# Kernel tuning notes

Hardware: AMD Instinct MI355X
Metric: run time of the kernel (lower is better)

Reference implementation:

```python
import jax, jax.numpy as jnp
import numpy as np
import math

B, S = 512, 100
L, U = 50000, 2000
D, LOC_DIM, USER_DIM, TEMP_DIM = 80, 56, 12, 12
NHEAD, DFF = 4, 160


def _pe(seq_len, d):
    pos = np.arange(seq_len, dtype=np.float32)[:, None]
    div = np.exp(np.arange(0, d, 2, dtype=np.float32) * (-math.log(10000.0) / d))
    pe = np.zeros((seq_len, d), dtype=np.float32)
    pe[:, 0::2] = np.sin(pos * div)
    pe[:, 1::2] = np.cos(pos * div)
    return jnp.asarray(pe)


def _ln(x, g, b, eps=1e-5):
    m = x.mean(-1, keepdims=True)
    v = ((x - m) ** 2).mean(-1, keepdims=True)
    return (x - m) * jax.lax.rsqrt(v + eps) * g + b


def setup_inputs():
    key = jax.random.key(0)
    ks = jax.random.split(key, 16)
    f32 = jnp.float32
    def n(k, shape, s):
        return (jax.random.normal(k, shape) * s).astype(f32)
    return {
        'loc_seq': jax.random.randint(ks[0], (B, S), 0, L),
        'user_seq': jax.random.randint(ks[1], (B, S), 0, U),
        'weekday_seq': jax.random.randint(ks[2], (B, S), 0, 7),
        'start_min_seq': (jax.random.uniform(ks[3], (B, S)) * 1440.0).astype(f32),
        'dur_seq': (jax.random.uniform(ks[4], (B, S)) * 120.0).astype(f32),
        'diff_seq': jax.random.randint(ks[5], (B, S), 0, 7),
        'mask': jnp.ones((B, S), dtype=bool),
        'loc_emb': n(ks[6], (L, LOC_DIM), 0.01).at[0].set(0.0),
        'user_emb': n(ks[7], (U, USER_DIM), 0.01).at[0].set(0.0),
        'Wt': n(ks[8], (6, TEMP_DIM), 0.3), 'bt': jnp.zeros((TEMP_DIM,), f32),
        'in_g': jnp.ones((D,), f32), 'in_b': jnp.zeros((D,), f32),
        'Wq': n(ks[9], (D, D), 0.05), 'bq': jnp.zeros((D,), f32),
        'Wk': n(ks[10], (D, D), 0.05), 'bk': jnp.zeros((D,), f32),
        'Wv': n(ks[11], (D, D), 0.05), 'bv': jnp.zeros((D,), f32),
        'Wo': n(ks[12], (D, D), 0.05), 'bo': jnp.zeros((D,), f32),
        'ln1_g': jnp.ones((D,), f32), 'ln1_b': jnp.zeros((D,), f32),
        'W1': n(ks[13], (D, DFF), 0.05), 'b1': jnp.zeros((DFF,), f32),
        'W2': n(ks[14], (DFF, D), 0.05), 'b2': jnp.zeros((D,), f32),
        'ln2_g': jnp.ones((D,), f32), 'ln2_b': jnp.zeros((D,), f32),
        'out_g': jnp.ones((D,), f32), 'out_b': jnp.zeros((D,), f32),
        'Wp': n(ks[15], (D, L), 0.05), 'bp': jnp.zeros((L,), f32),
        'recency_decay': jnp.array(0.62, f32),
        'freq_weight': jnp.array(2.2, f32),
        'history_scale': jnp.array(11.0, f32),
        'model_weight': jnp.array(0.22, f32),
    }


def reference(loc_seq, user_seq, weekday_seq, start_min_seq, dur_seq, diff_seq, mask,
              loc_emb, user_emb, Wt, bt, in_g, in_b,
              Wq, bq, Wk, bk, Wv, bv, Wo, bo, ln1_g, ln1_b,
              W1, b1, W2, b2, ln2_g, ln2_b, out_g, out_b, Wp, bp,
              recency_decay, freq_weight, history_scale, model_weight):
    b, s = loc_seq.shape
    nloc = Wp.shape[1]
    valid = mask.astype(jnp.float32)
    # --- history scores: the torch per-timestep scatter loop, vectorized ---
    t = jnp.arange(s)
    rec_w = recency_decay ** (s - 1 - t).astype(jnp.float32)      # (s,) decay^time_from_end
    bidx = jnp.broadcast_to(jnp.arange(b)[:, None], (b, s))
    recency = jnp.zeros((b, nloc), jnp.float32).at[bidx, loc_seq].max(rec_w[None, :] * valid)
    freq = jnp.zeros((b, nloc), jnp.float32).at[bidx, loc_seq].add(valid)
    freq = freq / jnp.maximum(freq.max(axis=1, keepdims=True), 1.0)
    history_scores = history_scale * (recency + freq_weight * freq)
    # --- embeddings & temporal features ---
    time_rad = start_min_seq / 60.0 / 24.0 * 2.0 * math.pi
    wd_rad = weekday_seq.astype(jnp.float32) / 7.0 * 2.0 * math.pi
    feats = jnp.stack([jnp.sin(time_rad), jnp.cos(time_rad), jnp.log1p(dur_seq) / 8.0,
                       jnp.sin(wd_rad), jnp.cos(wd_rad), diff_seq.astype(jnp.float32) / 7.0], axis=-1)
    x = jnp.concatenate([loc_emb[loc_seq], user_emb[user_seq], feats @ Wt + bt], axis=-1)
    x = _ln(x, in_g, in_b) + _pe(s, x.shape[-1])[None]
    # --- 1-layer post-norm transformer encoder, erf-gelu, eval (no dropout) ---
    dh = D // NHEAD
    q = (x @ Wq + bq).reshape(b, s, NHEAD, dh)
    k = (x @ Wk + bk).reshape(b, s, NHEAD, dh)
    v = (x @ Wv + bv).reshape(b, s, NHEAD, dh)
    scores = jnp.einsum('bqhd,bkhd->bhqk', q, k) / math.sqrt(dh)
    scores = jnp.where(mask[:, None, None, :], scores, -1e9)
    attn = jnp.einsum('bhqk,bkhd->bqhd', jax.nn.softmax(scores, axis=-1), v).reshape(b, s, D)
    x = _ln(x + attn @ Wo + bo, ln1_g, ln1_b)
    x = _ln(x + jax.nn.gelu(x @ W1 + b1, approximate=False) @ W2 + b2, ln2_g, ln2_b)
    # --- gather last valid position ---
    last_idx = mask.sum(axis=1) - 1
    last = jnp.take_along_axis(x, last_idx[:, None, None], axis=1)[:, 0]
    last = _ln(last, out_g, out_b)
    learned = jax.nn.softmax(last @ Wp + bp, axis=1) * nloc
    return history_scores + model_weight * learned
```

## Files before the change

### kernel.cpp

```cpp
#include <hip/hip_runtime.h>
#include <hip/hip_bf16.h>
#include <math.h>

#define B 512
#define S 100
#define L 50000
#define D 80
#define NHEAD 4
#define DH 20
#define DFF 160
#define NTOK (B*S)
#define NTILES 3125

typedef __attribute__((ext_vector_type(8))) short bf16x8v;
typedef __attribute__((ext_vector_type(4))) float f32x4v;
typedef __attribute__((ext_vector_type(4))) unsigned short u16x4;
typedef __attribute__((ext_vector_type(8))) unsigned short u16x8;

__device__ __forceinline__ unsigned short f2bf(float f) {
    unsigned int x = __float_as_uint(f);
    unsigned int r = (x + 0x7FFFu + ((x >> 16) & 1u)) >> 16;
    return (unsigned short)r;
}

__device__ __forceinline__ float bf2f(unsigned short u) {
    return __uint_as_float(((unsigned int)u) << 16);
}

__device__ __forceinline__ float pe_val(int s, int d) {
    int k = d >> 1;
    float ang = (float)s * expf(-0.23025850929940458f * (float)k);
    return (d & 1) ? cosf(ang) : sinf(ang);
}

__global__ __launch_bounds__(256) void pack_all(const float* __restrict__ Wq, const float* __restrict__ Wk,
                        const float* __restrict__ Wv, const float* __restrict__ Wo,
                        const float* __restrict__ W1, const float* __restrict__ W2,
                        unsigned short* __restrict__ U) {
    int bid = blockIdx.x;
    const float* W; int K, N, KT, nt; unsigned short* dst;
    if (bid < 15)      { int mt = bid / 5; nt = bid % 5; W = (mt==0)?Wq:(mt==1)?Wk:Wv; K=80; N=80; KT=3; dst = U + (size_t)bid * 1536; }
    else if (bid < 20) { nt = bid - 15; W = Wo; K=80;  N=80;  KT=3; dst = U + 23040 + (size_t)nt * 1536; }
    else if (bid < 30) { nt = bid - 20; W = W1; K=80;  N=160; KT=3; dst = U + 30720 + (size_t)nt * 1536; }
    else               { nt = bid - 30; W = W2; K=160; N=80;  KT=5; dst = U + 46080 + (size_t)nt * 2560; }
    int total = KT * 512;
    for (int idx = threadIdx.x; idx < total; idx += 256) {
        int j = idx & 7, n = (idx >> 3) & 15, q = (idx >> 7) & 3, kt = idx >> 9;
        int k = kt * 32 + q * 8 + j;
        float val = (k < K) ? W[(size_t)k * N + nt * 16 + n] : 0.f;
        dst[idx] = f2bf(val);
    }
}

__global__ __launch_bounds__(256) void build_x(const int* __restrict__ loc_seq, const int* __restrict__ user_seq,
                        const int* __restrict__ weekday_seq, const float* __restrict__ start_min,
                        const float* __restrict__ dur, const int* __restrict__ diff,
                        const float* __restrict__ loc_emb, const float* __restrict__ user_emb,
                        const float* __restrict__ Wt, const float* __restrict__ bt,
                        const float* __restrict__ in_g, const float* __restrict__ in_b,
                        unsigned short* __restrict__ x) {
    int token = blockIdx.x * 4 + (threadIdx.x >> 6);
    int lane = threadIdx.x & 63;
    int s = token % S;
    int lidx = loc_seq[token];
    int uidx = user_seq[token];
    float tr = start_min[token] * (2.f * (float)M_PI / 1440.f);
    float wd = (float)weekday_seq[token] * (2.f * (float)M_PI / 7.f);
    float f0 = sinf(tr), f1 = cosf(tr);
    float f2 = log1pf(dur[token]) * 0.125f;
    float f3 = sinf(wd), f4 = cosf(wd);
    float f5 = (float)diff[token] * (1.f / 7.f);
    float v1;
    if (lane < 56) v1 = loc_emb[(size_t)lidx * 56 + lane];
    else           v1 = user_emb[(size_t)uidx * 12 + (lane - 56)];
    float v2 = 0.f;
    if (lane < 4) {
        v2 = user_emb[(size_t)uidx * 12 + 8 + lane];
    } else if (lane < 16) {
        int j = lane - 4;
        v2 = bt[j] + f0 * Wt[j] + f1 * Wt[12 + j] + f2 * Wt[24 + j]
                   + f3 * Wt[36 + j] + f4 * Wt[48 + j] + f5 * Wt[60 + j];
    }
    float sum = v1 + v2, sq = v1 * v1 + v2 * v2;
    #pragma unroll
    for (int off = 1; off < 64; off <<= 1) {
        sum += __shfl_xor(sum, off);
        sq  += __shfl_xor(sq,  off);
    }
    float mean = sum * 0.0125f;
    float var = sq * 0.0125f - mean * mean;
    float rstd = rsqrtf(var + 1e-5f);
    x[(size_t)token * D + lane] = f2bf((v1 - mean) * rstd * in_g[lane] + in_b[lane] + pe_val(s, lane));
    if (lane < 16) {
        int d2 = 64 + lane;
        x[(size_t)token * D + d2] = f2bf((v2 - mean) * rstd * in_g[d2] + in_b[d2] + pe_val(s, d2));
    }
}

__global__ __launch_bounds__(512) void qkv_attn_last(const unsigned short* __restrict__ xg,
      const unsigned short* __restrict__ qkvP,
      const float* __restrict__ bq, const float* __restrict__ bk, const float* __restrict__ bv,
      unsigned short* __restrict__ ao_last) {
    __shared__ __align__(16) unsigned short xbf[112 * 96];
    __shared__ __align__(16) unsigned short kls[112 * 128];
    __shared__ __align__(16) unsigned short vt[4 * 32 * 128];
    __shared__ __align__(16) unsigned short qls[16 * 128];
    __shared__ float pls[4 * 112];
    __shared__ float lls[4];
    int tid = threadIdx.x;
    int b = blockIdx.x;
    size_t base = (size_t)b * (S * D);
    f32x4v zz = {0.f, 0.f, 0.f, 0.f};
    f32x4v* k4 = (f32x4v*)kls; f32x4v* v4 = (f32x4v*)vt; f32x4v* q4 = (f32x4v*)qls;
    #pragma unroll
    for (int ii = 0; ii < 4; ++ii) { int i = tid + ii * 512; if (i < 1792) k4[i] = zz; }
    #pragma unroll
    for (int ii = 0; ii < 4; ++ii) v4[tid + ii * 512] = zz;
    if (tid < 256) q4[tid] = zz;
    #pragma unroll
    for (int ii = 0; ii < 4; ++ii) {
        int i = tid + ii * 512;
        if (i < 2000) {
            int row = i / 20, c0 = (i % 20) * 4;
            *(u16x4*)&xbf[row * 96 + c0] = *(const u16x4*)&xg[base + row * 80 + c0];
        }
    }
    unsigned int* xb32 = (unsigned int*)xbf;
    for (int i = tid; i < 576; i += 512) xb32[4800 + i] = 0;
    for (int i = tid; i < 800; i += 512) { int r = i / 8, c = i % 8; xb32[r * 48 + 40 + c] = 0; }
    __syncthreads();
    int w = tid >> 6, lane = tid & 63;
    int qd = lane >> 4, m = lane & 15;
    if (w < 7) {
        int mt = w;
        bf16x8v a[3];
        #pragma unroll
        for (int t = 0; t < 3; ++t)
            a[t] = *(const bf16x8v*)&xbf[(mt * 16 + m) * 96 + t * 32 + qd * 8];
        #pragma unroll
        for (int nt = 0; nt < 15; ++nt) {
            f32x4v acc = {0.f, 0.f, 0.f, 0.f};
            #pragma unroll
            for (int t = 0; t < 3; ++t) {
                bf16x8v bb = *(const bf16x8v*)&qkvP[(((size_t)(nt * 3 + t)) * 4 + qd) * 128 + m * 8];
                acc = __builtin_amdgcn_mfma_f32_16x16x32_bf16(a[t], bb, acc, 0, 0, 0);
            }
            int mat = nt / 5;
            int col80 = nt * 16 + m - mat * 80;
            int h = col80 / 20, dd = col80 % 20;
            const float* bias = (mat == 0) ? bq : (mat == 1) ? bk : bv;
            float bbv = bias[col80];
            float scl = (mat == 0) ? 0.22360679774997896f : 1.f;
            #pragma unroll
            for (int r = 0; r < 4; ++r) {
                int row = mt * 16 + qd * 4 + r;
                unsigned short val = f2bf((acc[r] + bbv) * scl);
                if (mat == 0) {
                    if (row >= 96) qls[(row - 96) * 128 + ((h * 32 + dd) ^ ((row & 7) << 3))] = val;
                } else if (mat == 1) {
                    kls[row * 128 + ((h * 32 + dd) ^ ((row & 7) << 3))] = val;
                } else {
                    vt[h * 4096 + dd * 128 + (row ^ ((dd & 7) << 3))] = val;
                }
            }
        }
    }
    __syncthreads();
    if (w < 4) {
        int hb = w * 32;
        bf16x8v aq = *(const bf16x8v*)&qls[m * 128 + ((hb + qd * 8) ^ ((m & 7) << 3))];
        f32x4v scv[7];
        #pragma unroll
        for (int nt = 0; nt < 7; ++nt) {
            int krow = nt * 16 + m;
            bf16x8v bk_ = *(const bf16x8v*)&kls[krow * 128 + ((hb + qd * 8) ^ ((krow & 7) << 3))];
            f32x4v z = {0.f, 0.f, 0.f, 0.f};
            scv[nt] = __builtin_amdgcn_mfma_f32_16x16x32_bf16(aq, bk_, z, 0, 0, 0);
        }
        float mx = scv[0][3];
        #pragma unroll
        for (int nt = 1; nt < 6; ++nt) mx = fmaxf(mx, scv[nt][3]);
        float s6 = scv[6][3];
        if (m < 4) mx = fmaxf(mx, s6);
        #pragma unroll
        for (int off = 1; off < 16; off <<= 1) mx = fmaxf(mx, __shfl_xor(mx, off));
        float p[7], l = 0.f;
        #pragma unroll
        for (int nt = 0; nt < 6; ++nt) { p[nt] = expf(scv[nt][3] - mx); l += p[nt]; }
        p[6] = (m < 4) ? expf(s6 - mx) : 0.f; l += p[6];
        #pragma unroll
        for (int off = 1; off < 16; off <<= 1) l += __shfl_xor(l, off);
        if (qd == 0) {
            #pragma unroll
            for (int nt = 0; nt < 7; ++nt) pls[w * 112 + nt * 16 + m] = p[nt];
            if (m == 0) lls[w] = l;
        }
    }
    __syncthreads();
    if (w < 4 && lane < 20) {
        float invl = 1.f / lls[w];
        int dsw = (lane & 7) << 3;
        float acc = 0.f;
        #pragma unroll 4
        for (int s = 0; s < 100; ++s)
            acc += pls[w * 112 + s] * bf2f(vt[w * 4096 + lane * 128 + (s ^ dsw)]);
        ao_last[(size_t)b * 80 + w * 20 + lane] = f2bf(acc * invl);
    }
}

__global__ __launch_bounds__(256) void tail_kern(const unsigned short* __restrict__ ao_last,
      const unsigned short* __restrict__ xg,
      const unsigned short* __restrict__ woP, const float* __restrict__ bo,
      const float* __restrict__ ln1g, const float* __restrict__ ln1b,
      const unsigned short* __restrict__ w1P, const float* __restrict__ b1,
      const unsigned short* __restrict__ w2P, const float* __restrict__ b2,
      const float* __restrict__ ln2g, const float* __restrict__ ln2b,
      const float* __restrict__ outg, const float* __restrict__ outb,
      unsigned short* __restrict__ apack) {
    __shared__ unsigned short ubuf[64 * 160];
    __shared__ unsigned short xbf[64 * 96];
    __shared__ float ys[64 * 84];
    __shared__ float rsum[64][4], rsq[64][4];
    __shared__ float mstat[64], rstat[64];
    int tid = threadIdx.x;
    int b0 = blockIdx.x * 64;
    #pragma unroll
    for (int ii = 0; ii < 5; ++ii) {
        int i = tid + ii * 256;
        int row = i / 20, c0 = (i % 20) * 4;
        *(u16x4*)&ubuf[row * 96 + c0] = *(const u16x4*)&ao_last[(size_t)(b0 + row) * 80 + c0];
        u16x4 xv = *(const u16x4*)&xg[((size_t)(b0 + row) * S + (S - 1)) * 80 + c0];
        f32x4v xf;
        #pragma unroll
        for (int j = 0; j < 4; ++j) xf[j] = bf2f(xv[j]);
        *(f32x4v*)&ys[row * 84 + c0] = xf;
    }
    #pragma unroll
    for (int ii = 0; ii < 2; ++ii) {
        int i = tid + ii * 256;
        int row = i >> 3, c = i & 7;
        ((unsigned int*)ubuf)[row * 48 + 40 + c] = 0;
    }
    __syncthreads();
    int w = tid >> 6, lane = tid & 63;
    int qd = lane >> 4, m = lane & 15;
    {
        bf16x8v a[3];
        #pragma unroll
        for (int t = 0; t < 3; ++t)
            a[t] = *(const bf16x8v*)&ubuf[(w * 16 + m) * 96 + t * 32 + qd * 8];
        #pragma unroll
        for (int nt = 0; nt < 5; ++nt) {
            f32x4v acc = {0.f, 0.f, 0.f, 0.f};
            #pragma unroll
            for (int t = 0; t < 3; ++t) {
                bf16x8v b = *(const bf16x8v*)&woP[(((size_t)(nt * 3 + t)) * 4 + qd) * 128 + m * 8];
                acc = __builtin_amdgcn_mfma_f32_16x16x32_bf16(a[t], b, acc, 0, 0, 0);
            }
            int col = nt * 16 + m;
            float bbv = bo[col];
            #pragma unroll
            for (int r = 0; r < 4; ++r)
                ys[(w * 16 + qd * 4 + r) * 84 + col] += acc[r] + bbv;
        }
    }
    __syncthreads();
    {
        int row = tid >> 2, qq = tid & 3;
        float s = 0.f, sq = 0.f;
        #pragma unroll
        for (int j = 0; j < 20; ++j) { float v = ys[row * 84 + qq + 4 * j]; s += v; sq += v * v; }
        rsum[row][qq] = s; rsq[row][qq] = sq;
    }
    __syncthreads();
    if (tid < 64) {
        float s = rsum[tid][0] + rsum[tid][1] + rsum[tid][2] + rsum[tid][3];
        float sq = rsq[tid][0] + rsq[tid][1] + rsq[tid][2] + rsq[tid][3];
        float mean = s * 0.0125f;
        float var = sq * 0.0125f - mean * mean;
        mstat[tid] = mean; rstat[tid] = rsqrtf(var + 1e-5f);
    }
    __syncthreads();
    for (int idx = tid; idx < 64 * 96; idx += 256) {
        int row = idx / 96, kk = idx % 96;
        float val = 0.f;
        if (kk < D) {
            val = (ys[row * 84 + kk] - mstat[row]) * rstat[row] * ln1g[kk] + ln1b[kk];
            ys[row * 84 + kk] = val;
        }
        xbf[idx] = f2bf(val);
    }
    __syncthreads();
    {
        bf16x8v a[3];
        #pragma unroll
        for (int t = 0; t < 3; ++t)
            a[t] = *(const bf16x8v*)&xbf[(w * 16 + m) * 96 + t * 32 + qd * 8];
        #pragma unroll
        for (int nt = 0; nt < 10; ++nt) {
            f32x4v acc = {0.f, 0.f, 0.f, 0.f};
            #pragma unroll
            for (int t = 0; t < 3; ++t) {
                bf16x8v b = *(const bf16x8v*)&w1P[(((size_t)(nt * 3 + t)) * 4 + qd) * 128 + m * 8];
                acc = __builtin_amdgcn_mfma_f32_16x16x32_bf16(a[t], b, acc, 0, 0, 0);
            }
            int col = nt * 16 + m;
            float bbv = b1[col];
            #pragma unroll
            for (int r = 0; r < 4; ++r) {
                float aa = acc[r] + bbv;
                float gl = 0.5f * aa * (1.f + erff(aa * 0.70710678118654752f));
                ubuf[(w * 16 + qd * 4 + r) * 160 + col] = f2bf(gl);
            }
        }
    }
    __syncthreads();
    {
        bf16x8v a2[5];
        #pragma unroll
        for (int t = 0; t < 5; ++t)
            a2[t] = *(const bf16x8v*)&ubuf[(w * 16 + m) * 160 + t * 32 + qd * 8];
        #pragma unroll
        for (int nt = 0; nt < 5; ++nt) {
            f32x4v acc = {0.f, 0.f, 0.f, 0.f};
            #pragma unroll
            for (int t = 0; t < 5; ++t) {
                bf16x8v b = *(const bf16x8v*)&w2P[(((size_t)(nt * 5 + t)) * 4 + qd) * 128 + m * 8];
                acc = __builtin_amdgcn_mfma_f32_16x16x32_bf16(a2[t], b, acc, 0, 0, 0);
            }
            int col = nt * 16 + m;
            float bbv = b2[col];
            #pragma unroll
            for (int r = 0; r < 4; ++r)
                ys[(w * 16 + qd * 4 + r) * 84 + col] += acc[r] + bbv;
        }
    }
    __syncthreads();
    {
        int row = tid >> 2, qq = tid & 3;
        float s = 0.f, sq = 0.f;
        #pragma unroll
        for (int j = 0; j < 20; ++j) { float v = ys[row * 84 + qq + 4 * j]; s += v; sq += v * v; }
        rsum[row][qq] = s; rsq[row][qq] = sq;
    }
    __syncthreads();
    if (tid < 64) {
        float s = rsum[tid][0] + rsum[tid][1] + rsum[tid][2] + rsum[tid][3];
        float sq = rsq[tid][0] + rsq[tid][1] + rsq[tid][2] + rsq[tid][3];
        float mean = s * 0.0125f;
        float var = sq * 0.0125f - mean * mean;
        mstat[tid] = mean; rstat[tid] = rsqrtf(var + 1e-5f);
    }
    __syncthreads();
    for (int idx = tid; idx < 64 * 80; idx += 256) {
        int row = idx / 80, col = idx % 80;
        ys[row * 84 + col] = (ys[row * 84 + col] - mstat[row]) * rstat[row] * ln2g[col] + ln2b[col];
    }
    __syncthreads();
    {
        int row = tid >> 2, qq = tid & 3;
        float s = 0.f, sq = 0.f;
        #pragma unroll
        for (int j = 0; j < 20; ++j) { float v = ys[row * 84 + qq + 4 * j]; s += v; sq += v * v; }
        rsum[row][qq] = s; rsq[row][qq] = sq;
    }
    __syncthreads();
    if (tid < 64) {
        float s = rsum[tid][0] + rsum[tid][1] + rsum[tid][2] + rsum[tid][3];
        float sq = rsq[tid][0] + rsq[tid][1] + rsq[tid][2] + rsq[tid][3];
        float mean = s * 0.0125f;
        float var = sq * 0.0125f - mean * mean;
        mstat[tid] = mean; rstat[tid] = rsqrtf(var + 1e-5f);
    }
    __syncthreads();
    for (int idx = tid; idx < 64 * 96; idx += 256) {
        int row = idx / 96, d = idx % 96;
        float val = 0.f;
        if (d < 80) val = (ys[row * 84 + d] - mstat[row]) * rstat[row] * outg[d] + outb[d];
        int bb = b0 + row;
        int mtile = bb >> 4, mm = bb & 15;
        int t = d >> 5, q = (d & 31) >> 3, j = d & 7;
        apack[((((size_t)mtile * 3 + t) * 4 + q) * 16 + mm) * 8 + j] = f2bf(val);
    }
}

__global__ __launch_bounds__(256) void wp_pack(const float* __restrict__ Wp, unsigned short* __restrict__ bpack,
                                               float* __restrict__ rowsum) {
    int tid = threadIdx.x;
    int nt = blockIdx.x;
    if (nt == 0) { rowsum[tid] = 0.f; rowsum[256 + tid] = 0.f; }
    for (int idx = tid; idx < 1536; idx += 256) {
        int n = idx & 15, kk = idx >> 4;
        int t = kk >> 5, q = (kk & 31) >> 3, j = kk & 7;
        float val = (kk < D) ? Wp[(size_t)kk * L + nt * 16 + n] : 0.f;
        bpack[((((size_t)nt * 3 + t) * 4 + q) * 16 + n) * 8 + j] = f2bf(val);
    }
}

__global__ __launch_bounds__(256) void rowsum_mfma(const unsigned short* __restrict__ apack,
                                                   const unsigned short* __restrict__ bpack,
                                                   const float* __restrict__ bp,
                                                   float* __restrict__ rowsum) {
    __shared__ float part[4][512];
    int tid = threadIdx.x;
    int w = tid >> 6, lane = tid & 63;
    int q = lane >> 4, m = lane & 15;
    int nt0 = (blockIdx.x * 4 + w) * 4;
    const bf16x8v* BP = (const bf16x8v*)bpack;
    const bf16x8v* AP = (const bf16x8v*)apack;
    bf16x8v bfr[4][3];
    float bpv[4], liv[4];
    #pragma unroll
    for (int i = 0; i < 4; ++i) {
        int ntile = nt0 + i;
        int ntc = ntile < NTILES ? ntile : NTILES - 1;
        liv[i] = ntile < NTILES ? 1.f : 0.f;
        #pragma unroll
        for (int t = 0; t < 3; ++t)
            bfr[i][t] = BP[((size_t)ntc * 3 + t) * 64 + q * 16 + m];
        bpv[i] = bp[ntc * 16 + m];
    }
    for (int mt = 0; mt < 32; ++mt) {
        bf16x8v a[3];
        #pragma unroll
        for (int t = 0; t < 3; ++t) a[t] = AP[((size_t)mt * 3 + t) * 64 + q * 16 + m];
        float rs[4] = {0.f, 0.f, 0.f, 0.f};
        #pragma unroll
        for (int i = 0; i < 4; ++i) {
            f32x4v acc = {0.f, 0.f, 0.f, 0.f};
            #pragma unroll
            for (int t = 0; t < 3; ++t)
                acc = __builtin_amdgcn_mfma_f32_16x16x32_bf16(a[t], bfr[i][t], acc, 0, 0, 0);
            #pragma unroll
            for (int r = 0; r < 4; ++r) rs[r] += liv[i] * expf(acc[r] + bpv[i]);
        }
        #pragma unroll
        for (int r = 0; r < 4; ++r) {
            #pragma unroll
            for (int off = 1; off < 16; off <<= 1) rs[r] += __shfl_xor(rs[r], off);
        }
        if (m == 0) {
            #pragma unroll
            for (int r = 0; r < 4; ++r) part[w][mt * 16 + q * 4 + r] = rs[r];
        }
    }
    __syncthreads();
    for (int i = tid; i < 512; i += 256) {
        float s = part[0][i] + part[1][i] + part[2][i] + part[3][i];
        atomicAdd(&rowsum[i], s);
    }
}

__global__ __launch_bounds__(256) void logits_final(const unsigned short* __restrict__ apack,
      const unsigned short* __restrict__ bpack, const float* __restrict__ bp,
      const float* __restrict__ rowsum, const float* __restrict__ mwp,
      float* __restrict__ out) {
    __shared__ float tile[2][16][68];
    __shared__ float sc[512];
    int tid = threadIdx.x;
    int w = tid >> 6, lane = tid & 63;
    int q = lane >> 4, m = lane & 15;
    float mwL = mwp[0] * (float)L;
    for (int i = tid; i < 512; i += 256) sc[i] = mwL / rowsum[i];
    int ntile = blockIdx.x * 4 + w;
    int ntc = ntile < NTILES ? ntile : NTILES - 1;
    bool live = ntile < NTILES;
    const bf16x8v* BP = (const bf16x8v*)bpack;
    const bf16x8v* AP = (const bf16x8v*)apack;
    bf16x8v bfr[3];
    #pragma unroll
    for (int t = 0; t < 3; ++t) bfr[t] = BP[((size_t)ntc * 3 + t) * 64 + q * 16 + m];
    float bpv = bp[ntc * 16 + m];
    int row = tid >> 4, c4 = tid & 15;
    int gc = blockIdx.x * 64 + c4 * 4;
    bool cok = gc + 4 <= L;
    bf16x8v aC[3], aN[3];
    #pragma unroll
    for (int t = 0; t < 3; ++t) aC[t] = AP[(size_t)t * 64 + q * 16 + m];
    __syncthreads();
    for (int mt = 0; mt < 32; ++mt) {
        if (mt < 31) {
            #pragma unroll
            for (int t = 0; t < 3; ++t) aN[t] = AP[((size_t)(mt + 1) * 3 + t) * 64 + q * 16 + m];
        }
        f32x4v acc = {0.f, 0.f, 0.f, 0.f};
        #pragma unroll
        for (int t = 0; t < 3; ++t)
            acc = __builtin_amdgcn_mfma_f32_16x16x32_bf16(aC[t], bfr[t], acc, 0, 0, 0);
        int buf = mt & 1;
        if (live) {
            #pragma unroll
            for (int r = 0; r < 4; ++r)
                tile[buf][q * 4 + r][w * 16 + m] = expf(acc[r] + bpv);
        }
        __syncthreads();
        if (cok) {
            float4 v = *(float4*)&tile[buf][row][c4 * 4];
            float s = sc[mt * 16 + row];
            v.x *= s; v.y *= s; v.z *= s; v.w *= s;
            *(float4*)&out[(size_t)(mt * 16 + row) * L + gc] = v;
        }
        #pragma unroll
        for (int t = 0; t < 3; ++t) aC[t] = aN[t];
    }
}

__global__ void history_kern(const int* __restrict__ loc_seq, const float* __restrict__ decp,
                             const float* __restrict__ fwp, const float* __restrict__ hsp,
                             float* __restrict__ out) {
    int b = blockIdx.x;
    int t = threadIdx.x;
    __shared__ int locs[S];
    __shared__ float red[128];
    if (t < S) locs[t] = loc_seq[(size_t)b * S + t];
    __syncthreads();
    int cnt = 0;
    bool isLast = false;
    int myloc = -1;
    if (t < S) {
        myloc = locs[t];
        isLast = true;
        for (int u = 0; u < S; ++u) {
            if (locs[u] == myloc) { cnt++; if (u > t) isLast = false; }
        }
    }
    red[t] = (float)cnt;
    __syncthreads();
    for (int off = 64; off; off >>= 1) { if (t < off) red[t] = fmaxf(red[t], red[t + off]); __syncthreads(); }
    float denom = fmaxf(red[0], 1.0f);
    if (t < S && isLast) {
        float rec = powf(decp[0], (float)(S - 1 - t));
        out[(size_t)b * L + myloc] += hsp[0] * (rec + fwp[0] * (float)cnt / denom);
    }
}

extern "C" void kernel_launch(void* const* d_in, const int* in_sizes, int n_in,
                              void* d_out, int out_size, void* d_ws, size_t ws_size,
                              hipStream_t stream) {
    (void)in_sizes; (void)n_in; (void)out_size; (void)ws_size;
    const int*   loc_seq   = (const int*)  d_in[0];
    const int*   user_seq  = (const int*)  d_in[1];
    const int*   weekday   = (const int*)  d_in[2];
    const float* start_min = (const float*)d_in[3];
    const float* dur       = (const float*)d_in[4];
    const int*   diff      = (const int*)  d_in[5];
    const float* loc_emb = (const float*)d_in[7];
    const float* user_emb= (const float*)d_in[8];
    const float* Wt  = (const float*)d_in[9];  const float* bt  = (const float*)d_in[10];
    const float* in_g= (const float*)d_in[11]; const float* in_b= (const float*)d_in[12];
    const float* Wq  = (const float*)d_in[13]; const float* bq  = (const float*)d_in[14];
    const float* Wk  = (const float*)d_in[15]; const float* bk  = (const float*)d_in[16];
    const float* Wv  = (const float*)d_in[17]; const float* bv  = (const float*)d_in[18];
    const float* Wo  = (const float*)d_in[19]; const float* bo  = (const float*)d_in[20];
    const float* ln1g= (const float*)d_in[21]; const float* ln1b= (const float*)d_in[22];
    const float* W1  = (const float*)d_in[23]; const float* b1  = (const float*)d_in[24];
    const float* W2  = (const float*)d_in[25]; const float* b2  = (const float*)d_in[26];
    const float* ln2g= (const float*)d_in[27]; const float* ln2b= (const float*)d_in[28];
    const float* outg= (const float*)d_in[29]; const float* outb= (const float*)d_in[30];
    const float* Wp  = (const float*)d_in[31]; const float* bp  = (const float*)d_in[32];
    const float* dec = (const float*)d_in[33]; const float* fw  = (const float*)d_in[34];
    const float* hs  = (const float*)d_in[35]; const float* mw  = (const float*)d_in[36];

    float* ws   = (float*)d_ws;
    unsigned short* Xb = (unsigned short*)ws;
    unsigned short* APACK = (unsigned short*)(ws + 4096000);
    float* RSUM = ws + 20480000;
    unsigned short* WPACKS = (unsigned short*)(ws + 20481000);
    unsigned short* QKVP = WPACKS;
    unsigned short* WOP  = WPACKS + 23040;
    unsigned short* W1P  = WPACKS + 30720;
    unsigned short* W2P  = WPACKS + 46080;
    unsigned short* AOL  = WPACKS + 60000;
    unsigned short* BPACK = (unsigned short*)(ws + 16384000);
    float* out  = (float*)d_out;

    pack_all<<<35, 256, 0, stream>>>(Wq, Wk, Wv, Wo, W1, W2, WPACKS);
    build_x<<<NTOK / 4, 256, 0, stream>>>(loc_seq, user_seq, weekday, start_min, dur, diff,
                                          loc_emb, user_emb, Wt, bt, in_g, in_b, Xb);
    qkv_attn_last<<<B, 512, 0, stream>>>(Xb, QKVP, bq, bk, bv, AOL);
    tail_kern<<<B / 64, 256, 0, stream>>>(AOL, Xb, WOP, bo, ln1g, ln1b,
                                          W1P, b1, W2P, b2, ln2g, ln2b,
                                          outg, outb, APACK);
    wp_pack<<<NTILES, 256, 0, stream>>>(Wp, BPACK, RSUM);
    rowsum_mfma<<<(NTILES + 15) / 16, 256, 0, stream>>>(APACK, BPACK, bp, RSUM);
    logits_final<<<(NTILES + 3) / 4, 256, 0, stream>>>(APACK, BPACK, bp, RSUM, mw, out);
    history_kern<<<B, 128, 0, stream>>>(loc_seq, dec, fw, hs, out);
}
```

Before: 343.0 us.

## Fuse embedding build into attention kernel and merge weight packing launches

The embedding gather, temporal features, input layernorm and positional encoding are now computed directly into shared memory inside the attention kernel, so the full bf16 activation tensor is no longer written to and re-read from global memory. Only the last-position row is written out for the tail kernel. The Wp packing is merged with the small weight packing into one launch, removing two kernel launches in total. expf is also swapped for the fast __expf in the logits kernels, which trades a little accuracy for cheaper exponentials.

```diff
diff --git a/kernel.cpp b/kernel.cpp
--- a/kernel.cpp
+++ b/kernel.cpp
@@ -33,74 +33,49 @@
     return (d & 1) ? cosf(ang) : sinf(ang);
 }
 
-__global__ __launch_bounds__(256) void pack_all(const float* __restrict__ Wq, const float* __restrict__ Wk,
+__global__ __launch_bounds__(256) void pack_kern(const float* __restrict__ Wq, const float* __restrict__ Wk,
                         const float* __restrict__ Wv, const float* __restrict__ Wo,
                         const float* __restrict__ W1, const float* __restrict__ W2,
-                        unsigned short* __restrict__ U) {
+                        const float* __restrict__ Wp,
+                        unsigned short* __restrict__ U, unsigned short* __restrict__ bpack,
+                        float* __restrict__ rowsum) {
     int bid = blockIdx.x;
-    const float* W; int K, N, KT, nt; unsigned short* dst;
-    if (bid < 15)      { int mt = bid / 5; nt = bid % 5; W = (mt==0)?Wq:(mt==1)?Wk:Wv; K=80; N=80; KT=3; dst = U + (size_t)bid * 1536; }
-    else if (bid < 20) { nt = bid - 15; W = Wo; K=80;  N=80;  KT=3; dst = U + 23040 + (size_t)nt * 1536; }
-    else if (bid < 30) { nt = bid - 20; W = W1; K=80;  N=160; KT=3; dst = U + 30720 + (size_t)nt * 1536; }
-    else               { nt = bid - 30; W = W2; K=160; N=80;  KT=5; dst = U + 46080 + (size_t)nt * 2560; }
-    int total = KT * 512;
-    for (int idx = threadIdx.x; idx < total; idx += 256) {
-        int j = idx & 7, n = (idx >> 3) & 15, q = (idx >> 7) & 3, kt = idx >> 9;
-        int k = kt * 32 + q * 8 + j;
-        float val = (k < K) ? W[(size_t)k * N + nt * 16 + n] : 0.f;
-        dst[idx] = f2bf(val);
-    }
-}
-
-__global__ __launch_bounds__(256) void build_x(const int* __restrict__ loc_seq, const int* __restrict__ user_seq,
-                        const int* __restrict__ weekday_seq, const float* __restrict__ start_min,
-                        const float* __restrict__ dur, const int* __restrict__ diff,
-                        const float* __restrict__ loc_emb, const float* __restrict__ user_emb,
-                        const float* __restrict__ Wt, const float* __restrict__ bt,
-                        const float* __restrict__ in_g, const float* __restrict__ in_b,
-                        unsigned short* __restrict__ x) {
-    int token = blockIdx.x * 4 + (threadIdx.x >> 6);
-    int lane = threadIdx.x & 63;
-    int s = token % S;
-    int lidx = loc_seq[token];
-    int uidx = user_seq[token];
-    float tr = start_min[token] * (2.f * (float)M_PI / 1440.f);
-    float wd = (float)weekday_seq[token] * (2.f * (float)M_PI / 7.f);
-    float f0 = sinf(tr), f1 = cosf(tr);
-    float f2 = log1pf(dur[token]) * 0.125f;
-    float f3 = sinf(wd), f4 = cosf(wd);
-    float f5 = (float)diff[token] * (1.f / 7.f);
-    float v1;
-    if (lane < 56) v1 = loc_emb[(size_t)lidx * 56 + lane];
-    else           v1 = user_emb[(size_t)uidx * 12 + (lane - 56)];
-    float v2 = 0.f;
-    if (lane < 4) {
-        v2 = user_emb[(size_t)uidx * 12 + 8 + lane];
-    } else if (lane < 16) {
-        int j = lane - 4;
-        v2 = bt[j] + f0 * Wt[j] + f1 * Wt[12 + j] + f2 * Wt[24 + j]
-                   + f3 * Wt[36 + j] + f4 * Wt[48 + j] + f5 * Wt[60 + j];
-    }
-    float sum = v1 + v2, sq = v1 * v1 + v2 * v2;
-    #pragma unroll
-    for (int off = 1; off < 64; off <<= 1) {
-        sum += __shfl_xor(sum, off);
-        sq  += __shfl_xor(sq,  off);
-    }
-    float mean = sum * 0.0125f;
-    float var = sq * 0.0125f - mean * mean;
-    float rstd = rsqrtf(var + 1e-5f);
-    x[(size_t)token * D + lane] = f2bf((v1 - mean) * rstd * in_g[lane] + in_b[lane] + pe_val(s, lane));
-    if (lane < 16) {
-        int d2 = 64 + lane;
-        x[(size_t)token * D + d2] = f2bf((v2 - mean) * rstd * in_g[d2] + in_b[d2] + pe_val(s, d2));
-    }
-}
-
-__global__ __launch_bounds__(512) void qkv_attn_last(const unsigned short* __restrict__ xg,
+    int tid = threadIdx.x;
+    if (bid < 35) {
+        if (bid == 0) { rowsum[tid] = 0.f; rowsum[256 + tid] = 0.f; }
+        const float* W; int K, N, KT, nt; unsigned short* dst;
+        if (bid < 15)      { int mt = bid / 5; nt = bid % 5; W = (mt==0)?Wq:(mt==1)?Wk:Wv; K=80; N=80; KT=3; dst = U + (size_t)bid * 1536; }
+        else if (bid < 20) { nt = bid - 15; W = Wo; K=80;  N=80;  KT=3; dst = U + 23040 + (size_t)nt * 1536; }
+        else if (bid < 30) { nt = bid - 20; W = W1; K=80;  N=160; KT=3; dst = U + 30720 + (size_t)nt * 1536; }
+        else               { nt = bid - 30; W = W2; K=160; N=80;  KT=5; dst = U + 46080 + (size_t)nt * 2560; }
+        int total = KT * 512;
+        for (int idx = tid; idx < total; idx += 256) {
+            int j = idx & 7, n = (idx >> 3) & 15, q = (idx >> 7) & 3, kt = idx >> 9;
+            int k = kt * 32 + q * 8 + j;
+            float val = (k < K) ? W[(size_t)k * N + nt * 16 + n] : 0.f;
+            dst[idx] = f2bf(val);
+        }
+    } else {
+        int nt = bid - 35;
+        for (int idx = tid; idx < 1536; idx += 256) {
+            int n = idx & 15, kk = idx >> 4;
+            int t = kk >> 5, q = (kk & 31) >> 3, j = kk & 7;
+            float val = (kk < D) ? Wp[(size_t)kk * L + nt * 16 + n] : 0.f;
+            bpack[((((size_t)nt * 3 + t) * 4 + q) * 16 + n) * 8 + j] = f2bf(val);
+        }
+    }
+}
+
+__global__ __launch_bounds__(512) void qkv_attn_last(
+      const int* __restrict__ loc_seq, const int* __restrict__ user_seq,
+      const int* __restrict__ weekday_seq, const float* __restrict__ start_min,
+      const float* __restrict__ dur, const int* __restrict__ diff,
+      const float* __restrict__ loc_emb, const float* __restrict__ user_emb,
+      const float* __restrict__ Wt, const float* __restrict__ bt,
+      const float* __restrict__ in_g, const float* __restrict__ in_b,
       const unsigned short* __restrict__ qkvP,
       const float* __restrict__ bq, const float* __restrict__ bk, const float* __restrict__ bv,
-      unsigned short* __restrict__ ao_last) {
+      unsigned short* __restrict__ ao_last, unsigned short* __restrict__ x_last) {
     __shared__ __align__(16) unsigned short xbf[112 * 96];
     __shared__ __align__(16) unsigned short kls[112 * 128];
     __shared__ __align__(16) unsigned short vt[4 * 32 * 128];
@@ -109,7 +84,6 @@
     __shared__ float lls[4];
     int tid = threadIdx.x;
     int b = blockIdx.x;
-    size_t base = (size_t)b * (S * D);
     f32x4v zz = {0.f, 0.f, 0.f, 0.f};
     f32x4v* k4 = (f32x4v*)kls; f32x4v* v4 = (f32x4v*)vt; f32x4v* q4 = (f32x4v*)qls;
     #pragma unroll
@@ -117,20 +91,60 @@
     #pragma unroll
     for (int ii = 0; ii < 4; ++ii) v4[tid + ii * 512] = zz;
     if (tid < 256) q4[tid] = zz;
-    #pragma unroll
-    for (int ii = 0; ii < 4; ++ii) {
-        int i = tid + ii * 512;
-        if (i < 2000) {
-            int row = i / 20, c0 = (i % 20) * 4;
-            *(u16x4*)&xbf[row * 96 + c0] = *(const u16x4*)&xg[base + row * 80 + c0];
-        }
-    }
     unsigned int* xb32 = (unsigned int*)xbf;
     for (int i = tid; i < 576; i += 512) xb32[4800 + i] = 0;
     for (int i = tid; i < 800; i += 512) { int r = i / 8, c = i % 8; xb32[r * 48 + 40 + c] = 0; }
-    __syncthreads();
     int w = tid >> 6, lane = tid & 63;
     int qd = lane >> 4, m = lane & 15;
+    for (int it = 0; it < 13; ++it) {
+        int s = w + it * 8;
+        if (s < 100) {
+            int token = b * S + s;
+            int lidx = loc_seq[token];
+            int uidx = user_seq[token];
+            float tr = start_min[token] * (2.f * (float)M_PI / 1440.f);
+            float wd = (float)weekday_seq[token] * (2.f * (float)M_PI / 7.f);
+            float f0 = sinf(tr), f1 = cosf(tr);
+            float f2 = log1pf(dur[token]) * 0.125f;
+            float f3 = sinf(wd), f4 = cosf(wd);
+            float f5 = (float)diff[token] * (1.f / 7.f);
+            float v1;
+            if (lane < 56) v1 = loc_emb[(size_t)lidx * 56 + lane];
+            else           v1 = user_emb[(size_t)uidx * 12 + (lane - 56)];
+            float v2 = 0.f;
+            if (lane < 4) {
+                v2 = user_emb[(size_t)uidx * 12 + 8 + lane];
+            } else if (lane < 16) {
+                int j = lane - 4;
+                v2 = bt[j] + f0 * Wt[j] + f1 * Wt[12 + j] + f2 * Wt[24 + j]
+                           + f3 * Wt[36 + j] + f4 * Wt[48 + j] + f5 * Wt[60 + j];
+            }
+            float sum = v1 + v2, sq = v1 * v1 + v2 * v2;
+            #pragma unroll
+            for (int off = 1; off < 64; off <<= 1) {
+                sum += __shfl_xor(sum, off);
+                sq  += __shfl_xor(sq,  off);
+            }
+            float mean = sum * 0.0125f;
+            float var = sq * 0.0125f - mean * mean;
+            float rstd = rsqrtf(var + 1e-5f);
+            float o1 = (v1 - mean) * rstd * in_g[lane] + in_b[lane] + pe_val(s, lane);
+            unsigned short o1b = f2bf(o1);
+            xbf[s * 96 + lane] = o1b;
+            unsigned short o2b = 0;
+            if (lane < 16) {
+                int d2 = 64 + lane;
+                float o2 = (v2 - mean) * rstd * in_g[d2] + in_b[d2] + pe_val(s, d2);
+                o2b = f2bf(o2);
+                xbf[s * 96 + d2] = o2b;
+            }
+            if (s == S - 1) {
+                x_last[(size_t)b * 80 + lane] = o1b;
+                if (lane < 16) x_last[(size_t)b * 80 + 64 + lane] = o2b;
+            }
+        }
+    }
+    __syncthreads();
     if (w < 7) {
         int mt = w;
         bf16x8v a[3];
@@ -209,7 +223,7 @@
 }
 
 __global__ __launch_bounds__(256) void tail_kern(const unsigned short* __restrict__ ao_last,
-      const unsigned short* __restrict__ xg,
+      const unsigned short* __restrict__ x_last,
       const unsigned short* __restrict__ woP, const float* __restrict__ bo,
       const float* __restrict__ ln1g, const float* __restrict__ ln1b,
       const unsigned short* __restrict__ w1P, const float* __restrict__ b1,
@@ -229,7 +243,7 @@
         int i = tid + ii * 256;
         int row = i / 20, c0 = (i % 20) * 4;
         *(u16x4*)&ubuf[row * 96 + c0] = *(const u16x4*)&ao_last[(size_t)(b0 + row) * 80 + c0];
-        u16x4 xv = *(const u16x4*)&xg[((size_t)(b0 + row) * S + (S - 1)) * 80 + c0];
+        u16x4 xv = *(const u16x4*)&x_last[(size_t)(b0 + row) * 80 + c0];
         f32x4v xf;
         #pragma unroll
         for (int j = 0; j < 4; ++j) xf[j] = bf2f(xv[j]);
@@ -381,19 +395,6 @@
         int mtile = bb >> 4, mm = bb & 15;
         int t = d >> 5, q = (d & 31) >> 3, j = d & 7;
         apack[((((size_t)mtile * 3 + t) * 4 + q) * 16 + mm) * 8 + j] = f2bf(val);
-    }
-}
-
-__global__ __launch_bounds__(256) void wp_pack(const float* __restrict__ Wp, unsigned short* __restrict__ bpack,
-                                               float* __restrict__ rowsum) {
-    int tid = threadIdx.x;
-    int nt = blockIdx.x;
-    if (nt == 0) { rowsum[tid] = 0.f; rowsum[256 + tid] = 0.f; }
-    for (int idx = tid; idx < 1536; idx += 256) {
-        int n = idx & 15, kk = idx >> 4;
-        int t = kk >> 5, q = (kk & 31) >> 3, j = kk & 7;
-        float val = (kk < D) ? Wp[(size_t)kk * L + nt * 16 + n] : 0.f;
-        bpack[((((size_t)nt * 3 + t) * 4 + q) * 16 + n) * 8 + j] = f2bf(val);
     }
 }
 
@@ -432,7 +433,7 @@
             for (int t = 0; t < 3; ++t)
                 acc = __builtin_amdgcn_mfma_f32_16x16x32_bf16(a[t], bfr[i][t], acc, 0, 0, 0);
             #pragma unroll
-            for (int r = 0; r < 4; ++r) rs[r] += liv[i] * expf(acc[r] + bpv[i]);
+            for (int r = 0; r < 4; ++r) rs[r] += liv[i] * __expf(acc[r] + bpv[i]);
         }
         #pragma unroll
         for (int r = 0; r < 4; ++r) {
@@ -491,7 +492,7 @@
         if (live) {
             #pragma unroll
             for (int r = 0; r < 4; ++r)
-                tile[buf][q * 4 + r][w * 16 + m] = expf(acc[r] + bpv);
+                tile[buf][q * 4 + r][w * 16 + m] = __expf(acc[r] + bpv);
         }
         __syncthreads();
         if (cok) {
@@ -562,8 +563,8 @@
     const float* hs  = (const float*)d_in[35]; const float* mw  = (const float*)d_in[36];
 
     float* ws   = (float*)d_ws;
-    unsigned short* Xb = (unsigned short*)ws;
     unsigned short* APACK = (unsigned short*)(ws + 4096000);
+    unsigned short* BPACK = (unsigned short*)(ws + 16384000);
     float* RSUM = ws + 20480000;
     unsigned short* WPACKS = (unsigned short*)(ws + 20481000);
     unsigned short* QKVP = WPACKS;
@@ -571,17 +572,16 @@
     unsigned short* W1P  = WPACKS + 30720;
     unsigned short* W2P  = WPACKS + 46080;
     unsigned short* AOL  = WPACKS + 60000;
-    unsigned short* BPACK = (unsigned short*)(ws + 16384000);
+    unsigned short* XL   = WPACKS + 102400;
     float* out  = (float*)d_out;
 
-    pack_all<<<35, 256, 0, stream>>>(Wq, Wk, Wv, Wo, W1, W2, WPACKS);
-    build_x<<<NTOK / 4, 256, 0, stream>>>(loc_seq, user_seq, weekday, start_min, dur, diff,
-                                          loc_emb, user_emb, Wt, bt, in_g, in_b, Xb);
-    qkv_attn_last<<<B, 512, 0, stream>>>(Xb, QKVP, bq, bk, bv, AOL);
-    tail_kern<<<B / 64, 256, 0, stream>>>(AOL, Xb, WOP, bo, ln1g, ln1b,
+    pack_kern<<<35 + NTILES, 256, 0, stream>>>(Wq, Wk, Wv, Wo, W1, W2, Wp, WPACKS, BPACK, RSUM);
+    qkv_attn_last<<<B, 512, 0, stream>>>(loc_seq, user_seq, weekday, start_min, dur, diff,
+                                         loc_emb, user_emb, Wt, bt, in_g, in_b,
+                                         QKVP, bq, bk, bv, AOL, XL);
+    tail_kern<<<B / 64, 256, 0, stream>>>(AOL, XL, WOP, bo, ln1g, ln1b,
                                           W1P, b1, W2P, b2, ln2g, ln2b,
                                           outg, outb, APACK);
-    wp_pack<<<NTILES, 256, 0, stream>>>(Wp, BPACK, RSUM);
     rowsum_mfma<<<(NTILES + 15) / 16, 256, 0, stream>>>(APACK, BPACK, bp, RSUM);
     logits_final<<<(NTILES + 3) / 4, 256, 0, stream>>>(APACK, BPACK, bp, RSUM, mw, out);
     history_kern<<<B, 128, 0, stream>>>(loc_seq, dec, fw, hs, out);
```

New measurement: 336.7 us. About the same (-1.8%).
